# Kernel tuning notes

Hardware: AMD Instinct MI355X
Metric: run time of the kernel (lower is better)

The kernel has to match this reference:

```python
import jax, jax.numpy as jnp
import numpy as np

N = 50000      # num vertices
M = 10000      # num hyperedges
NNZ = 1600000  # incidence list length (avg degree 32)
D = 128        # in_features == out_features


def setup_inputs() -> dict:
    key = jax.random.key(0)
    k0, k1, k2, k3, k4, k5 = jax.random.split(key, 6)
    X = jax.random.normal(k0, (N, D), dtype=jnp.float32)
    X0 = jax.random.normal(k1, (N, D), dtype=jnp.float32)
    vertex = jax.random.randint(k2, (NNZ,), 0, N)
    edges = jax.random.randint(k3, (NNZ,), 0, M)
    # nn.Linear(D, D, bias=False) weight, kaiming-uniform-ish scale
    W = jax.random.uniform(k4, (D, D), dtype=jnp.float32,
                           minval=-1.0, maxval=1.0) / np.float32(np.sqrt(D))
    alpha = jax.random.uniform(k5, (), dtype=jnp.float32)
    beta = jnp.float32(0.5)
    return {"X": X, "X0": X0, "W": W, "alpha": alpha, "beta": beta,
            "vertex": vertex, "edges": edges}


def _scatter_mean(vals, idx, num_segments):
    # segment mean; empty segments -> 0 (matches torch_scatter 'mean')
    s = jax.ops.segment_sum(vals, idx, num_segments=num_segments)
    cnt = jax.ops.segment_sum(jnp.ones(idx.shape, vals.dtype), idx,
                              num_segments=num_segments)
    return s / jnp.maximum(cnt, 1.0)[:, None]


def reference(X, X0, W, alpha, beta, vertex, edges):
    Xve = X[vertex]                          # [NNZ, D] gather vertex -> incidence
    Xe = _scatter_mean(Xve, edges, M)        # [M, D]   hyperedge features
    Xev = Xe[edges]                          # [NNZ, D] gather edge -> incidence
    Xv = _scatter_mean(Xev, vertex, N)       # [N, D]   back to vertices
    Xi = (1.0 - alpha) * Xv + alpha * X0     # initial-residual mix
    return (1.0 - beta) * Xi + beta * (Xi @ W.T)  # identity-map mix + linear
```

## Files before the change

### kernel.cpp

```cpp
#include <hip/hip_runtime.h>
#include <hip/hip_bf16.h>


#define DD 128
#define NV 50000
#define ME 10000

#define CHUNK 4096
#define NEB 157
#define NVB 196
#define PB_CAP 12288

typedef __hip_bfloat16 bf16;
typedef __attribute__((ext_vector_type(8))) short short8v;
typedef __attribute__((ext_vector_type(4))) float float4v;

#define OFF_XE    0
#define OFF_ELIST 2560000
#define OFF_VLIST 8960000
#define OFF_EPAIR 15360000
#define OFF_VPAIR 21760000
#define OFF_XB    15360000
#define OFF_VOFF  28160000
#define OFF_EOFF  28360064
#define OFF_CBH   28400128
#define OFF_GBE   28401664
#define OFF_GBV   28402304
#define OFF_GCE   28403136
#define OFF_GCV   28403776
#define OFF_FLAG  28404608
#define OFF_WF    28404624
#define WS_USED   28470160

__device__ __forceinline__ float bf2f(unsigned short s) {
    union { unsigned u; float f; } x; x.u = ((unsigned)s) << 16; return x.f;
}
__device__ __forceinline__ unsigned f2bfu(float x) {
    union { bf16 h; unsigned short u; } c; c.h = __float2bfloat16(x); return (unsigned)c.u;
}
__device__ __forceinline__ float loadf(const void* p, long long i, unsigned f32) {
    if (f32) return ((const float*)p)[i];
    return bf2f(((const unsigned short*)p)[i]);
}
__device__ __forceinline__ void acc8(const uint4& u, float* a) {
    a[0] += bf2f((unsigned short)(u.x & 0xFFFFu));
    a[1] += bf2f((unsigned short)(u.x >> 16));
    a[2] += bf2f((unsigned short)(u.y & 0xFFFFu));
    a[3] += bf2f((unsigned short)(u.y >> 16));
    a[4] += bf2f((unsigned short)(u.z & 0xFFFFu));
    a[5] += bf2f((unsigned short)(u.z >> 16));
    a[6] += bf2f((unsigned short)(u.w & 0xFFFFu));
    a[7] += bf2f((unsigned short)(u.w >> 16));
}

__global__ void detect_kernel(const void* X, const void* X0, const void* W,
                              const void* beta_p, unsigned* flags) {
    int t = threadIdx.x;
    const unsigned short* px[3] = {(const unsigned short*)X,
                                   (const unsigned short*)X0,
                                   (const unsigned short*)W};
    for (int k = 0; k < 3; k++) {
        int big = 0;
        for (int i = t; i < 256; i += 64) {
            unsigned e = (px[k][i] >> 7) & 0xFFu;
            if (e >= 0x90u) big++;
        }
        for (int s = 32; s > 0; s >>= 1) big += __shfl_down(big, s);
        if (t == 0) flags[k] = (big >= 4) ? 1u : 0u;
    }
    if (t == 0) {
        unsigned short b = *(const unsigned short*)beta_p;
        flags[3] = (b == 0x3F00u) ? 0u : 1u;
    }
}

__global__ void prep_w(const void* W, const void* beta_p,
                       const unsigned* __restrict__ flags,
                       unsigned short* __restrict__ Wfrag) {
    int b = blockIdx.x * 256 + threadIdx.x;
    if (b >= 2048) return;
    int lane = b & 63, kk = (b >> 6) & 3, ct = b >> 8;
    int nn = lane & 15, quad = lane >> 4;
    int c = ct * 16 + nn;
    int kbase = kk * 32 + quad * 8;
    unsigned fW = flags[2], fS = flags[3];
    float beta = loadf(beta_p, 0, fS);
    float omb = 1.f - beta;
    unsigned short hi[8], lo[8];
#pragma unroll
    for (int j = 0; j < 8; j++) {
        float wv = loadf(W, (long long)c * DD + kbase + j, fW);
        float v = beta * wv + ((kbase + j) == c ? omb : 0.f);
        unsigned short h = (unsigned short)f2bfu(v);
        hi[j] = h;
        lo[j] = (unsigned short)f2bfu(v - bf2f(h));
    }
    uint4 ph, pl;
    ph.x = (unsigned)hi[0] | ((unsigned)hi[1] << 16);
    ph.y = (unsigned)hi[2] | ((unsigned)hi[3] << 16);
    ph.z = (unsigned)hi[4] | ((unsigned)hi[5] << 16);
    ph.w = (unsigned)hi[6] | ((unsigned)hi[7] << 16);
    pl.x = (unsigned)lo[0] | ((unsigned)lo[1] << 16);
    pl.y = (unsigned)lo[2] | ((unsigned)lo[3] << 16);
    pl.z = (unsigned)lo[4] | ((unsigned)lo[5] << 16);
    pl.w = (unsigned)lo[6] | ((unsigned)lo[7] << 16);
    ((uint4*)Wfrag)[b] = ph;
    ((uint4*)Wfrag)[2048 + b] = pl;
}

__global__ __launch_bounds__(256) void conv_x(const void* __restrict__ X,
                                              unsigned short* __restrict__ Xb,
                                              const unsigned* __restrict__ flags) {
    if (!flags[0]) return;
    int i = blockIdx.x * 256 + threadIdx.x;
    if (i >= NV * DD / 8) return;
    const float4* p = (const float4*)X + (size_t)i * 2;
    float4 a = p[0], b = p[1];
    uint4 o;
    o.x = f2bfu(a.x) | (f2bfu(a.y) << 16);
    o.y = f2bfu(a.z) | (f2bfu(a.w) << 16);
    o.z = f2bfu(b.x) | (f2bfu(b.y) << 16);
    o.w = f2bfu(b.z) | (f2bfu(b.w) << 16);
    ((uint4*)Xb)[i] = o;
}

__global__ __launch_bounds__(256) void coarse_hist(const int* __restrict__ vertex,
                                                   const int* __restrict__ edges,
                                                   unsigned* __restrict__ cbh, int nnz) {
    __shared__ unsigned h[NEB + NVB];
    int t = threadIdx.x;
    for (int i = t; i < NEB + NVB; i += 256) h[i] = 0;
    __syncthreads();
    int stride = gridDim.x * 256;
    for (int i = blockIdx.x * 256 + t; i < nnz; i += stride) {
        atomicAdd(&h[edges[i] >> 6], 1u);
        atomicAdd(&h[NEB + (vertex[i] >> 8)], 1u);
    }
    __syncthreads();
    for (int i = t; i < NEB + NVB; i += 256) {
        unsigned v = h[i];
        if (v) atomicAdd(&cbh[i], v);
    }
}

__global__ void scan353(const unsigned* __restrict__ cbh,
                        unsigned* __restrict__ gbe, unsigned* __restrict__ gbv,
                        unsigned* __restrict__ gce, unsigned* __restrict__ gcv,
                        unsigned* __restrict__ voff, unsigned* __restrict__ eoff,
                        int nnz) {
    __shared__ unsigned s[512];
    int t = threadIdx.x;
    unsigned v = (t < NEB + NVB) ? cbh[t] : 0u;
    s[t] = v;
    __syncthreads();
    for (int st = 1; st < 512; st <<= 1) {
        unsigned u = (t >= st) ? s[t - st] : 0u;
        __syncthreads();
        s[t] += u;
        __syncthreads();
    }
    unsigned excl = s[t] - v;
    if (t < NEB) {
        gbe[t] = excl; gce[t] = excl;
    } else if (t < NEB + NVB) {
        unsigned base = s[NEB - 1];
        gbv[t - NEB] = excl - base;
        gcv[t - NEB] = excl - base;
    }
    if (t == 0) {
        gbe[NEB] = (unsigned)nnz;
        gbv[NVB] = (unsigned)nnz;
        eoff[ME] = (unsigned)nnz;
        voff[NV] = (unsigned)nnz;
    }
}

__global__ __launch_bounds__(256) void build_pairs(const int* __restrict__ vertex,
                                                   const int* __restrict__ edges,
                                                   unsigned* __restrict__ gcur_e,
                                                   unsigned* __restrict__ gcur_v,
                                                   unsigned* __restrict__ epairs,
                                                   unsigned* __restrict__ vpairs, int nnz) {
    __shared__ unsigned buf[CHUNK];
    __shared__ unsigned hist[256], scn[256], loff[256], cur[256], gbase[256];
    int t = threadIdx.x;
    int base = blockIdx.x * CHUNK;
    int len = min(CHUNK, nnz - base);
    if (len <= 0) return;

    for (int phase = 0; phase < 2; phase++) {
        int sh = phase ? 8 : 6;
        int nb = phase ? NVB : NEB;
        unsigned* gcur = phase ? gcur_v : gcur_e;
        unsigned* pairs = phase ? vpairs : epairs;
        if (phase) __syncthreads();
        hist[t] = 0;
        __syncthreads();
        for (int i = t; i < len; i += 256) {
            int key = phase ? vertex[base + i] : edges[base + i];
            atomicAdd(&hist[key >> sh], 1u);
        }
        __syncthreads();
        unsigned hv = hist[t];
        scn[t] = hv;
        __syncthreads();
        for (int st = 1; st < 256; st <<= 1) {
            unsigned u = (t >= st) ? scn[t - st] : 0u;
            __syncthreads();
            scn[t] += u;
            __syncthreads();
        }
        loff[t] = scn[t] - hv;
        cur[t] = scn[t] - hv;
        if (t < nb && hv > 0) gbase[t] = atomicAdd(&gcur[t], hv);
        __syncthreads();
        for (int i = t; i < len; i += 256) {
            int k = phase ? vertex[base + i] : edges[base + i];
            int v2 = phase ? edges[base + i] : vertex[base + i];
            unsigned pk = ((unsigned)k << 16) | (unsigned)v2;
            unsigned p = atomicAdd(&cur[k >> sh], 1u);
            buf[p] = pk;
        }
        __syncthreads();
        for (int i = t; i < len; i += 256) {
            unsigned pk = buf[i];
            unsigned b = (pk >> 16) >> sh;
            pairs[gbase[b] + (i - loff[b])] = pk;
        }
    }
}

__global__ __launch_bounds__(256) void build_lists(const unsigned* __restrict__ epairs,
                                                   const unsigned* __restrict__ vpairs,
                                                   const unsigned* __restrict__ gbe,
                                                   const unsigned* __restrict__ gbv,
                                                   unsigned* __restrict__ eoff,
                                                   unsigned* __restrict__ voff,
                                                   unsigned* __restrict__ elist,
                                                   unsigned* __restrict__ vlist) {
    __shared__ unsigned buf[PB_CAP];
    __shared__ unsigned offs[256], curs[256];
    int b = blockIdx.x, t = threadIdx.x;
    const unsigned* pairs;
    unsigned* off;
    unsigned* list;
    unsigned s0, s1;
    int k0, nk;
    if (b < NEB) {
        pairs = epairs; off = eoff; list = elist;
        k0 = b << 6; nk = min(64, ME - k0);
        s0 = gbe[b]; s1 = gbe[b + 1];
    } else {
        int bb = b - NEB;
        pairs = vpairs; off = voff; list = vlist;
        k0 = bb << 8; nk = min(256, NV - k0);
        s0 = gbv[bb]; s1 = gbv[bb + 1];
    }
    int len = (int)(s1 - s0);

    curs[t] = 0;
    __syncthreads();
    for (int i = t; i < len; i += 256) {
        unsigned pk = pairs[s0 + i];
        atomicAdd(&curs[(pk >> 16) - k0], 1u);
    }
    __syncthreads();
    unsigned hv = curs[t];
    offs[t] = hv;
    __syncthreads();
    for (int st = 1; st < 256; st <<= 1) {
        unsigned u = (t >= st) ? offs[t - st] : 0u;
        __syncthreads();
        offs[t] += u;
        __syncthreads();
    }
    unsigned my_excl = offs[t] - hv;
    __syncthreads();
    offs[t] = my_excl;
    curs[t] = 0;
    if (t < nk) off[k0 + t] = s0 + my_excl;
    __syncthreads();

    if (len <= PB_CAP) {
        for (int i = t; i < len; i += 256) {
            unsigned pk = pairs[s0 + i];
            int lk = (int)(pk >> 16) - k0;
            unsigned p = offs[lk] + atomicAdd(&curs[lk], 1u);
            buf[p] = pk & 0xFFFFu;
        }
        __syncthreads();
        for (int i = t; i < len; i += 256) list[s0 + i] = buf[i];
    } else {
        for (int i = t; i < len; i += 256) {
            unsigned pk = pairs[s0 + i];
            int lk = (int)(pk >> 16) - k0;
            unsigned p = offs[lk] + atomicAdd(&curs[lk], 1u);
            list[s0 + p] = pk & 0xFFFFu;
        }
    }
}

__global__ __launch_bounds__(256, 8) void edge_agg(const void* __restrict__ X,
                                                   const unsigned short* __restrict__ Xb,
                                                   const unsigned* __restrict__ eoff,
                                                   const unsigned* __restrict__ elist,
                                                   unsigned short* __restrict__ Xe,
                                                   const unsigned* __restrict__ flags, int m) {
    __shared__ float red[4][DD];
    int e = blockIdx.x;
    int t = threadIdx.x, lane = t & 63, w = t >> 6;
    const unsigned short* Xp = flags[0] ? Xb : (const unsigned short*)X;
    unsigned s0 = eoff[e], s1 = eoff[e + 1];
    float a[8];
#pragma unroll
    for (int i = 0; i < 8; i++) a[i] = 0.f;

    int sub = t & 15;
    unsigned q = s0 + (unsigned)(t >> 4);
    for (; q + 16 < s1; q += 32) {
        unsigned v0 = elist[q], v1 = elist[q + 16];
        uint4 u0 = *(const uint4*)(Xp + (size_t)v0 * DD + 8 * sub);
        uint4 u1 = *(const uint4*)(Xp + (size_t)v1 * DD + 8 * sub);
        acc8(u0, a); acc8(u1, a);
    }
    if (q < s1) {
        unsigned v0 = elist[q];
        uint4 u0 = *(const uint4*)(Xp + (size_t)v0 * DD + 8 * sub);
        acc8(u0, a);
    }
#pragma unroll
    for (int i = 0; i < 8; i++) {
        a[i] += __shfl_xor(a[i], 16);
        a[i] += __shfl_xor(a[i], 32);
    }
    if ((lane >> 4) == 0) {
#pragma unroll
        for (int i = 0; i < 8; i++) red[w][8 * sub + i] = a[i];
    }
    __syncthreads();
    if (t < DD) {
        float inv = (s1 > s0) ? 1.f / (float)(s1 - s0) : 1.f;
        float v = (red[0][t] + red[1][t] + red[2][t] + red[3][t]) * inv;
        Xe[(size_t)e * DD + t] = (unsigned short)f2bfu(v);
    }
}

__global__ __launch_bounds__(512, 6) void vertex_out(const unsigned short* __restrict__ Xe,
                                                     const unsigned* __restrict__ voff,
                                                     const unsigned* __restrict__ vlist,
                                                     const void* __restrict__ X0,
                                                     const unsigned short* __restrict__ Wfrag,
                                                     const void* __restrict__ alpha_p,
                                                     void* __restrict__ out,
                                                     const unsigned* __restrict__ flags, int n) {
    __shared__ short8v A_hi[512];
    __shared__ short8v A_lo[512];
    int t = threadIdx.x, lane = t & 63, w = t >> 6;
    unsigned fX = flags[0], f0 = flags[1], fS = flags[3];
    float alpha = loadf(alpha_p, 0, fS);
    float oma = 1.f - alpha;
    int v0 = blockIdx.x * 32;

    int g = lane >> 4, sub = lane & 15;
    for (int j = 0; j < 4; j++) {
        int r = w * 4 + j, v = v0 + r;
        int rt = r >> 4, mm = r & 15;
        int idx = (rt * 4 + (sub >> 2)) * 64 + (sub & 3) * 16 + mm;
        float a[8];
#pragma unroll
        for (int i = 0; i < 8; i++) a[i] = 0.f;
        if (v < n) {
            unsigned s0 = voff[v], s1 = voff[v + 1];
            unsigned q = s0;
            for (; q + 8 <= s1; q += 8) {
                unsigned e0 = vlist[q + g];
                unsigned e1 = vlist[q + 4 + g];
                uint4 u0 = *(const uint4*)(Xe + (size_t)e0 * DD + 8 * sub);
                uint4 u1 = *(const uint4*)(Xe + (size_t)e1 * DD + 8 * sub);
                acc8(u0, a); acc8(u1, a);
            }
            if (q + 4 <= s1) {
                unsigned e0 = vlist[q + g];
                uint4 u0 = *(const uint4*)(Xe + (size_t)e0 * DD + 8 * sub);
                acc8(u0, a);
                q += 4;
            }
            int rem = (int)(s1 - q);
            if (g < rem) {
                unsigned e0 = vlist[q + g];
                uint4 u0 = *(const uint4*)(Xe + (size_t)e0 * DD + 8 * sub);
                acc8(u0, a);
            }
#pragma unroll
            for (int i = 0; i < 8; i++) {
                a[i] += __shfl_xor(a[i], 16);
                a[i] += __shfl_xor(a[i], 32);
            }
            if (g == 0) {
                float inv = (s1 > s0) ? 1.f / (float)(s1 - s0) : 1.f;
                float x0[8];
                if (!f0) {
                    uint4 u = *(const uint4*)((const unsigned short*)X0 + (size_t)v * DD + 8 * sub);
                    x0[0] = bf2f((unsigned short)(u.x & 0xFFFFu));
                    x0[1] = bf2f((unsigned short)(u.x >> 16));
                    x0[2] = bf2f((unsigned short)(u.y & 0xFFFFu));
                    x0[3] = bf2f((unsigned short)(u.y >> 16));
                    x0[4] = bf2f((unsigned short)(u.z & 0xFFFFu));
                    x0[5] = bf2f((unsigned short)(u.z >> 16));
                    x0[6] = bf2f((unsigned short)(u.w & 0xFFFFu));
                    x0[7] = bf2f((unsigned short)(u.w >> 16));
                } else {
                    const float4* p = (const float4*)((const float*)X0 + (size_t)v * DD + 8 * sub);
                    float4 A = p[0], B = p[1];
                    x0[0] = A.x; x0[1] = A.y; x0[2] = A.z; x0[3] = A.w;
                    x0[4] = B.x; x0[5] = B.y; x0[6] = B.z; x0[7] = B.w;
                }
                short8v ah, al;
#pragma unroll
                for (int i = 0; i < 8; i++) {
                    float xi = oma * (a[i] * inv) + alpha * x0[i];
                    unsigned short h = (unsigned short)f2bfu(xi);
                    ah[i] = (short)h;
                    al[i] = (short)f2bfu(xi - bf2f(h));
                }
                A_hi[idx] = ah;
                A_lo[idx] = al;
            }
        } else if (g == 0) {
            short8v zf = {0, 0, 0, 0, 0, 0, 0, 0};
            A_hi[idx] = zf;
            A_lo[idx] = zf;
        }
    }

    __syncthreads();
    int rt = w & 1, ct = w >> 1;
    short8v ah[4], al[4];
#pragma unroll
    for (int kk = 0; kk < 4; kk++) {
        ah[kk] = A_hi[(rt * 4 + kk) * 64 + lane];
        al[kk] = A_lo[(rt * 4 + kk) * 64 + lane];
    }
    const short8v* Bh = (const short8v*)Wfrag;
    const short8v* Bl = Bh + 2048;
#pragma unroll
    for (int tt = 0; tt < 2; tt++) {
        int c2 = ct + 4 * tt;
        float4v acc = {0.f, 0.f, 0.f, 0.f};
#pragma unroll
        for (int kk = 0; kk < 4; kk++) {
            short8v bh = Bh[(c2 * 4 + kk) * 64 + lane];
            short8v bl = Bl[(c2 * 4 + kk) * 64 + lane];
            acc = __builtin_amdgcn_mfma_f32_16x16x32_bf16(ah[kk], bh, acc, 0, 0, 0);
            acc = __builtin_amdgcn_mfma_f32_16x16x32_bf16(al[kk], bh, acc, 0, 0, 0);
            acc = __builtin_amdgcn_mfma_f32_16x16x32_bf16(ah[kk], bl, acc, 0, 0, 0);
        }
        int col = c2 * 16 + (lane & 15);
        int rbase = v0 + rt * 16 + (lane >> 4) * 4;
#pragma unroll
        for (int reg = 0; reg < 4; reg++) {
            int row = rbase + reg;
            if (row < n) {
                if (fX) ((float*)out)[(size_t)row * DD + col] = acc[reg];
                else    ((bf16*)out)[(size_t)row * DD + col] = __float2bfloat16(acc[reg]);
            }
        }
    }
}

extern "C" void kernel_launch(void* const* d_in, const int* in_sizes, int n_in,
                              void* d_out, int out_size, void* d_ws, size_t ws_size,
                              hipStream_t stream) {
    const void* X      = d_in[0];
    const void* X0     = d_in[1];
    const void* W      = d_in[2];
    const void* alpha  = d_in[3];
    const void* beta   = d_in[4];
    const int*  vertex = (const int*)d_in[5];
    const int*  edges  = (const int*)d_in[6];
    const int nnz = in_sizes[5];

    char* ws = (char*)d_ws;
    unsigned short* Xe = (unsigned short*)(ws + OFF_XE);
    unsigned* elist  = (unsigned*)(ws + OFF_ELIST);
    unsigned* vlist  = (unsigned*)(ws + OFF_VLIST);
    unsigned* epairs = (unsigned*)(ws + OFF_EPAIR);
    unsigned* vpairs = (unsigned*)(ws + OFF_VPAIR);
    unsigned short* Xb = (unsigned short*)(ws + OFF_XB);
    unsigned* voff   = (unsigned*)(ws + OFF_VOFF);
    unsigned* eoff   = (unsigned*)(ws + OFF_EOFF);
    unsigned* cbh    = (unsigned*)(ws + OFF_CBH);
    unsigned* gbe    = (unsigned*)(ws + OFF_GBE);
    unsigned* gbv    = (unsigned*)(ws + OFF_GBV);
    unsigned* gce    = (unsigned*)(ws + OFF_GCE);
    unsigned* gcv    = (unsigned*)(ws + OFF_GCV);
    unsigned* flags  = (unsigned*)(ws + OFF_FLAG);
    unsigned short* Wfrag = (unsigned short*)(ws + OFF_WF);

    hipMemsetAsync(ws + OFF_CBH, 0, 1536, stream);

    detect_kernel<<<1, 64, 0, stream>>>(X, X0, W, beta, flags);

    prep_w<<<8, 256, 0, stream>>>(W, beta, flags, Wfrag);

    coarse_hist<<<512, 256, 0, stream>>>(vertex, edges, cbh, nnz);

    scan353<<<1, 512, 0, stream>>>(cbh, gbe, gbv, gce, gcv, voff, eoff, nnz);

    int pa_blocks = (nnz + CHUNK - 1) / CHUNK;
    build_pairs<<<pa_blocks, 256, 0, stream>>>(vertex, edges, gce, gcv,
                                               epairs, vpairs, nnz);

    build_lists<<<NEB + NVB, 256, 0, stream>>>(epairs, vpairs, gbe, gbv,
                                               eoff, voff, elist, vlist);

    conv_x<<<(NV * DD / 8 + 255) / 256, 256, 0, stream>>>(X, Xb, flags);

    edge_agg<<<ME, 256, 0, stream>>>(X, Xb, eoff, elist, Xe, flags, ME);

    vertex_out<<<(NV + 31) / 32, 512, 0, stream>>>(Xe, voff, vlist, X0, Wfrag,
                                                   alpha, d_out, flags, NV);
}
```

Measured before the change: 283.5 us.

## Fuse prep kernels, unroll gather loops, pad LDS, hoist X0 load

Merges the format-detect, weight-prep and coarse-histogram kernels into one launch. The weight-prep blocks now recompute the W format flag per wave, which removes the dependency on the separate detect kernel and saves two launches. Both gather loops, edge aggregation and vertex output, are unrolled to keep four row loads in flight. The LDS A tiles are padded to avoid bank conflicts, and the X0 load is issued before the edge-gather loop so its latency overlaps. The cost is more registers per thread and slightly more shared memory.

```diff
diff --git a/kernel.cpp b/kernel.cpp
--- a/kernel.cpp
+++ b/kernel.cpp
@@ -53,59 +53,96 @@
     a[7] += bf2f((unsigned short)(u.w >> 16));
 }
 
-__global__ void detect_kernel(const void* X, const void* X0, const void* W,
-                              const void* beta_p, unsigned* flags) {
-    int t = threadIdx.x;
-    const unsigned short* px[3] = {(const unsigned short*)X,
-                                   (const unsigned short*)X0,
-                                   (const unsigned short*)W};
-    for (int k = 0; k < 3; k++) {
-        int big = 0;
-        for (int i = t; i < 256; i += 64) {
-            unsigned e = (px[k][i] >> 7) & 0xFFu;
-            if (e >= 0x90u) big++;
-        }
-        for (int s = 32; s > 0; s >>= 1) big += __shfl_down(big, s);
-        if (t == 0) flags[k] = (big >= 4) ? 1u : 0u;
-    }
-    if (t == 0) {
-        unsigned short b = *(const unsigned short*)beta_p;
-        flags[3] = (b == 0x3F00u) ? 0u : 1u;
-    }
-}
-
-__global__ void prep_w(const void* W, const void* beta_p,
-                       const unsigned* __restrict__ flags,
-                       unsigned short* __restrict__ Wfrag) {
-    int b = blockIdx.x * 256 + threadIdx.x;
-    if (b >= 2048) return;
-    int lane = b & 63, kk = (b >> 6) & 3, ct = b >> 8;
-    int nn = lane & 15, quad = lane >> 4;
-    int c = ct * 16 + nn;
-    int kbase = kk * 32 + quad * 8;
-    unsigned fW = flags[2], fS = flags[3];
-    float beta = loadf(beta_p, 0, fS);
-    float omb = 1.f - beta;
-    unsigned short hi[8], lo[8];
-#pragma unroll
-    for (int j = 0; j < 8; j++) {
-        float wv = loadf(W, (long long)c * DD + kbase + j, fW);
-        float v = beta * wv + ((kbase + j) == c ? omb : 0.f);
-        unsigned short h = (unsigned short)f2bfu(v);
-        hi[j] = h;
-        lo[j] = (unsigned short)f2bfu(v - bf2f(h));
-    }
-    uint4 ph, pl;
-    ph.x = (unsigned)hi[0] | ((unsigned)hi[1] << 16);
-    ph.y = (unsigned)hi[2] | ((unsigned)hi[3] << 16);
-    ph.z = (unsigned)hi[4] | ((unsigned)hi[5] << 16);
-    ph.w = (unsigned)hi[6] | ((unsigned)hi[7] << 16);
-    pl.x = (unsigned)lo[0] | ((unsigned)lo[1] << 16);
-    pl.y = (unsigned)lo[2] | ((unsigned)lo[3] << 16);
-    pl.z = (unsigned)lo[4] | ((unsigned)lo[5] << 16);
-    pl.w = (unsigned)lo[6] | ((unsigned)lo[7] << 16);
-    ((uint4*)Wfrag)[b] = ph;
-    ((uint4*)Wfrag)[2048 + b] = pl;
+__device__ __forceinline__ unsigned wave_is_fp32(const unsigned short* p) {
+    int l = threadIdx.x & 63;
+    int big = 0;
+    for (int i = l; i < 256; i += 64) {
+        unsigned e = (p[i] >> 7) & 0xFFu;
+        if (e >= 0x90u) big++;
+    }
+    for (int s = 32; s > 0; s >>= 1) big += __shfl_down(big, s);
+    return (__shfl(big, 0) >= 4) ? 1u : 0u;
+}
+
+__global__ __launch_bounds__(256) void prep_all(const void* X, const void* X0, const void* W,
+                                                const void* beta_p,
+                                                const int* __restrict__ vertex,
+                                                const int* __restrict__ edges,
+                                                unsigned* __restrict__ flags,
+                                                unsigned short* __restrict__ Wfrag,
+                                                unsigned* __restrict__ cbh, int nnz) {
+    __shared__ unsigned h[NEB + NVB];
+    int b = blockIdx.x, t = threadIdx.x;
+
+    if (b == 0) {
+        if (t < 64) {
+            const unsigned short* px[3] = {(const unsigned short*)X,
+                                           (const unsigned short*)X0,
+                                           (const unsigned short*)W};
+            for (int k = 0; k < 3; k++) {
+                int big = 0;
+                for (int i = t; i < 256; i += 64) {
+                    unsigned e = (px[k][i] >> 7) & 0xFFu;
+                    if (e >= 0x90u) big++;
+                }
+                for (int s = 32; s > 0; s >>= 1) big += __shfl_down(big, s);
+                if (t == 0) flags[k] = (big >= 4) ? 1u : 0u;
+            }
+            if (t == 0) {
+                unsigned short bb = *(const unsigned short*)beta_p;
+                flags[3] = (bb == 0x3F00u) ? 0u : 1u;
+            }
+        }
+        return;
+    }
+
+    if (b <= 8) {
+        int blob = (b - 1) * 256 + t;
+        unsigned fW = wave_is_fp32((const unsigned short*)W);
+        unsigned short bu = *(const unsigned short*)beta_p;
+        unsigned fS = (bu == 0x3F00u) ? 0u : 1u;
+        int lane = blob & 63, kk = (blob >> 6) & 3, ct = blob >> 8;
+        int nn = lane & 15, quad = lane >> 4;
+        int c = ct * 16 + nn;
+        int kbase = kk * 32 + quad * 8;
+        float beta = loadf(beta_p, 0, fS);
+        float omb = 1.f - beta;
+        unsigned short hi[8], lo[8];
+#pragma unroll
+        for (int j = 0; j < 8; j++) {
+            float wv = loadf(W, (long long)c * DD + kbase + j, fW);
+            float v = beta * wv + ((kbase + j) == c ? omb : 0.f);
+            unsigned short hh = (unsigned short)f2bfu(v);
+            hi[j] = hh;
+            lo[j] = (unsigned short)f2bfu(v - bf2f(hh));
+        }
+        uint4 ph, pl;
+        ph.x = (unsigned)hi[0] | ((unsigned)hi[1] << 16);
+        ph.y = (unsigned)hi[2] | ((unsigned)hi[3] << 16);
+        ph.z = (unsigned)hi[4] | ((unsigned)hi[5] << 16);
+        ph.w = (unsigned)hi[6] | ((unsigned)hi[7] << 16);
+        pl.x = (unsigned)lo[0] | ((unsigned)lo[1] << 16);
+        pl.y = (unsigned)lo[2] | ((unsigned)lo[3] << 16);
+        pl.z = (unsigned)lo[4] | ((unsigned)lo[5] << 16);
+        pl.w = (unsigned)lo[6] | ((unsigned)lo[7] << 16);
+        ((uint4*)Wfrag)[blob] = ph;
+        ((uint4*)Wfrag)[2048 + blob] = pl;
+        return;
+    }
+
+    int hb = b - 9;
+    for (int i = t; i < NEB + NVB; i += 256) h[i] = 0;
+    __syncthreads();
+    int stride = 512 * 256;
+    for (int i = hb * 256 + t; i < nnz; i += stride) {
+        atomicAdd(&h[edges[i] >> 6], 1u);
+        atomicAdd(&h[NEB + (vertex[i] >> 8)], 1u);
+    }
+    __syncthreads();
+    for (int i = t; i < NEB + NVB; i += 256) {
+        unsigned v = h[i];
+        if (v) atomicAdd(&cbh[i], v);
+    }
 }
 
 __global__ __launch_bounds__(256) void conv_x(const void* __restrict__ X,
@@ -122,25 +159,6 @@
     o.z = f2bfu(b.x) | (f2bfu(b.y) << 16);
     o.w = f2bfu(b.z) | (f2bfu(b.w) << 16);
     ((uint4*)Xb)[i] = o;
-}
-
-__global__ __launch_bounds__(256) void coarse_hist(const int* __restrict__ vertex,
-                                                   const int* __restrict__ edges,
-                                                   unsigned* __restrict__ cbh, int nnz) {
-    __shared__ unsigned h[NEB + NVB];
-    int t = threadIdx.x;
-    for (int i = t; i < NEB + NVB; i += 256) h[i] = 0;
-    __syncthreads();
-    int stride = gridDim.x * 256;
-    for (int i = blockIdx.x * 256 + t; i < nnz; i += stride) {
-        atomicAdd(&h[edges[i] >> 6], 1u);
-        atomicAdd(&h[NEB + (vertex[i] >> 8)], 1u);
-    }
-    __syncthreads();
-    for (int i = t; i < NEB + NVB; i += 256) {
-        unsigned v = h[i];
-        if (v) atomicAdd(&cbh[i], v);
-    }
 }
 
 __global__ void scan353(const unsigned* __restrict__ cbh,
@@ -317,6 +335,15 @@
 
     int sub = t & 15;
     unsigned q = s0 + (unsigned)(t >> 4);
+    for (; q + 48 < s1; q += 64) {
+        unsigned v0 = elist[q], v1 = elist[q + 16];
+        unsigned v2 = elist[q + 32], v3 = elist[q + 48];
+        uint4 u0 = *(const uint4*)(Xp + (size_t)v0 * DD + 8 * sub);
+        uint4 u1 = *(const uint4*)(Xp + (size_t)v1 * DD + 8 * sub);
+        uint4 u2 = *(const uint4*)(Xp + (size_t)v2 * DD + 8 * sub);
+        uint4 u3 = *(const uint4*)(Xp + (size_t)v3 * DD + 8 * sub);
+        acc8(u0, a); acc8(u1, a); acc8(u2, a); acc8(u3, a);
+    }
     for (; q + 16 < s1; q += 32) {
         unsigned v0 = elist[q], v1 = elist[q + 16];
         uint4 u0 = *(const uint4*)(Xp + (size_t)v0 * DD + 8 * sub);
@@ -353,8 +380,8 @@
                                                      const void* __restrict__ alpha_p,
                                                      void* __restrict__ out,
                                                      const unsigned* __restrict__ flags, int n) {
-    __shared__ short8v A_hi[512];
-    __shared__ short8v A_lo[512];
+    __shared__ short8v A_hi[544];
+    __shared__ short8v A_lo[544];
     int t = threadIdx.x, lane = t & 63, w = t >> 6;
     unsigned fX = flags[0], f0 = flags[1], fS = flags[3];
     float alpha = loadf(alpha_p, 0, fS);
@@ -365,25 +392,37 @@
     for (int j = 0; j < 4; j++) {
         int r = w * 4 + j, v = v0 + r;
         int rt = r >> 4, mm = r & 15;
-        int idx = (rt * 4 + (sub >> 2)) * 64 + (sub & 3) * 16 + mm;
+        int idx = (rt * 4 + (sub >> 2)) * 68 + (sub & 3) * 17 + mm;
         float a[8];
 #pragma unroll
         for (int i = 0; i < 8; i++) a[i] = 0.f;
         if (v < n) {
             unsigned s0 = voff[v], s1 = voff[v + 1];
+            uint4 xu; float4 xA, xB;
+            if (g == 0) {
+                if (!f0) {
+                    xu = *(const uint4*)((const unsigned short*)X0 + (size_t)v * DD + 8 * sub);
+                } else {
+                    const float4* p = (const float4*)((const float*)X0 + (size_t)v * DD + 8 * sub);
+                    xA = p[0]; xB = p[1];
+                }
+            }
             unsigned q = s0;
-            for (; q + 8 <= s1; q += 8) {
+            for (; q + 16 <= s1; q += 16) {
                 unsigned e0 = vlist[q + g];
                 unsigned e1 = vlist[q + 4 + g];
+                unsigned e2 = vlist[q + 8 + g];
+                unsigned e3 = vlist[q + 12 + g];
                 uint4 u0 = *(const uint4*)(Xe + (size_t)e0 * DD + 8 * sub);
                 uint4 u1 = *(const uint4*)(Xe + (size_t)e1 * DD + 8 * sub);
-                acc8(u0, a); acc8(u1, a);
-            }
-            if (q + 4 <= s1) {
+                uint4 u2 = *(const uint4*)(Xe + (size_t)e2 * DD + 8 * sub);
+                uint4 u3 = *(const uint4*)(Xe + (size_t)e3 * DD + 8 * sub);
+                acc8(u0, a); acc8(u1, a); acc8(u2, a); acc8(u3, a);
+            }
+            for (; q + 4 <= s1; q += 4) {
                 unsigned e0 = vlist[q + g];
                 uint4 u0 = *(const uint4*)(Xe + (size_t)e0 * DD + 8 * sub);
                 acc8(u0, a);
-                q += 4;
             }
             int rem = (int)(s1 - q);
             if (g < rem) {
@@ -400,28 +439,25 @@
                 float inv = (s1 > s0) ? 1.f / (float)(s1 - s0) : 1.f;
                 float x0[8];
                 if (!f0) {
-                    uint4 u = *(const uint4*)((const unsigned short*)X0 + (size_t)v * DD + 8 * sub);
-                    x0[0] = bf2f((unsigned short)(u.x & 0xFFFFu));
-                    x0[1] = bf2f((unsigned short)(u.x >> 16));
-                    x0[2] = bf2f((unsigned short)(u.y & 0xFFFFu));
-                    x0[3] = bf2f((unsigned short)(u.y >> 16));
-                    x0[4] = bf2f((unsigned short)(u.z & 0xFFFFu));
-                    x0[5] = bf2f((unsigned short)(u.z >> 16));
-                    x0[6] = bf2f((unsigned short)(u.w & 0xFFFFu));
-                    x0[7] = bf2f((unsigned short)(u.w >> 16));
+                    x0[0] = bf2f((unsigned short)(xu.x & 0xFFFFu));
+                    x0[1] = bf2f((unsigned short)(xu.x >> 16));
+                    x0[2] = bf2f((unsigned short)(xu.y & 0xFFFFu));
+                    x0[3] = bf2f((unsigned short)(xu.y >> 16));
+                    x0[4] = bf2f((unsigned short)(xu.z & 0xFFFFu));
+                    x0[5] = bf2f((unsigned short)(xu.z >> 16));
+                    x0[6] = bf2f((unsigned short)(xu.w & 0xFFFFu));
+                    x0[7] = bf2f((unsigned short)(xu.w >> 16));
                 } else {
-                    const float4* p = (const float4*)((const float*)X0 + (size_t)v * DD + 8 * sub);
-                    float4 A = p[0], B = p[1];
-                    x0[0] = A.x; x0[1] = A.y; x0[2] = A.z; x0[3] = A.w;
-                    x0[4] = B.x; x0[5] = B.y; x0[6] = B.z; x0[7] = B.w;
+                    x0[0] = xA.x; x0[1] = xA.y; x0[2] = xA.z; x0[3] = xA.w;
+                    x0[4] = xB.x; x0[5] = xB.y; x0[6] = xB.z; x0[7] = xB.w;
                 }
                 short8v ah, al;
 #pragma unroll
                 for (int i = 0; i < 8; i++) {
                     float xi = oma * (a[i] * inv) + alpha * x0[i];
-                    unsigned short h = (unsigned short)f2bfu(xi);
-                    ah[i] = (short)h;
-                    al[i] = (short)f2bfu(xi - bf2f(h));
+                    unsigned short hh = (unsigned short)f2bfu(xi);
+                    ah[i] = (short)hh;
+                    al[i] = (short)f2bfu(xi - bf2f(hh));
                 }
                 A_hi[idx] = ah;
                 A_lo[idx] = al;
@@ -438,8 +474,9 @@
     short8v ah[4], al[4];
 #pragma unroll
     for (int kk = 0; kk < 4; kk++) {
-        ah[kk] = A_hi[(rt * 4 + kk) * 64 + lane];
-        al[kk] = A_lo[(rt * 4 + kk) * 64 + lane];
+        int ridx = (rt * 4 + kk) * 68 + (lane >> 4) * 17 + (lane & 15);
+        ah[kk] = A_hi[ridx];
+        al[kk] = A_lo[ridx];
     }
     const short8v* Bh = (const short8v*)Wfrag;
     const short8v* Bl = Bh + 2048;
@@ -499,11 +536,8 @@
 
     hipMemsetAsync(ws + OFF_CBH, 0, 1536, stream);
 
-    detect_kernel<<<1, 64, 0, stream>>>(X, X0, W, beta, flags);
-
-    prep_w<<<8, 256, 0, stream>>>(W, beta, flags, Wfrag);
-
-    coarse_hist<<<512, 256, 0, stream>>>(vertex, edges, cbh, nnz);
+    prep_all<<<521, 256, 0, stream>>>(X, X0, W, beta, vertex, edges,
+                                      flags, Wfrag, cbh, nnz);
 
     scan353<<<1, 512, 0, stream>>>(cbh, gbe, gbv, gce, gcv, voff, eoff, nnz);
 
```

Result: faster. 277.4 us (-2.2%).
